# Optimization experiments

Hardware: AMD Instinct MI355X
Metric: run time of the kernel (lower is better)

## Reference

```python
import jax, jax.numpy as jnp
import numpy as np

EMBED_DIM = 1024
N_HEADS = 16

def setup_inputs() -> dict:
    key = jax.random.key(0)
    ks = jax.random.split(key, 5)
    C = EMBED_DIM
    std = 1.0 / np.sqrt(C)
    x = jax.random.normal(ks[0], (2, 2048, C), dtype=jnp.float32)
    w_attn = jax.random.normal(ks[1], (C, 3 * C), dtype=jnp.float32) * std  # (in, out)
    b_attn = jax.random.normal(ks[2], (3 * C,), dtype=jnp.float32) * 0.01
    w_proj = jax.random.normal(ks[3], (C, C), dtype=jnp.float32) * std
    b_proj = jax.random.normal(ks[4], (C,), dtype=jnp.float32) * 0.01
    return {"x": x, "w_attn": w_attn, "b_attn": b_attn, "w_proj": w_proj, "b_proj": b_proj}

def reference(x, w_attn, b_attn, w_proj, b_proj):
    B, T, C = x.shape
    H = N_HEADS
    D = C // H
    qkv = x @ w_attn + b_attn                      # (B, T, 3C)
    q, k, v = jnp.split(qkv, 3, axis=2)
    # (B, T, C) -> (B, H, T, D)
    q = q.reshape(B, T, H, D).transpose(0, 2, 1, 3)
    k = k.reshape(B, T, H, D).transpose(0, 2, 1, 3)
    v = v.reshape(B, T, H, D).transpose(0, 2, 1, 3)
    # Faithful to source: query is divided by scale BEFORE QK^T, and the
    # similarity is divided by scale AGAIN before softmax (net scale = 1/D).
    scale = jnp.asarray(D, dtype=x.dtype) ** 0.5
    q = q / scale
    sim = jnp.einsum('bhnd,bhsd->bhns', q, k)      # (B, H, T, T)
    causal = jnp.tril(jnp.ones((T, T), dtype=bool))
    neg_min = jnp.finfo(sim.dtype).min
    sim = jnp.where(causal[None, None, :, :], sim, neg_min)
    attn = jax.nn.softmax(sim / scale, axis=-1)
    out = jnp.einsum('bhns,bhsd->bhnd', attn, v)   # (B, H, T, D)
    # source: gqa returns (b n h d), forward does transpose(1,2) -> (b h n d)
    # then .view(B, T, C); net effect is reshaping the (B,H,T,D) layout.
    y = out.reshape(B, T, C)
    y = y @ w_proj + b_proj
    return y
```

## Files before the change

kernel.cpp:

```cpp
#include <hip/hip_runtime.h>
#include <hip/hip_bf16.h>

#define BB 2
#define TT 2048
#define CC 1024
#define HH 16
#define DD 64
#define MM (BB*TT)
#define QSZ ((size_t)MM*CC)

#define QSCALE 0.022542110013890053f

typedef __attribute__((ext_vector_type(8))) short bf16x8;
typedef __attribute__((ext_vector_type(4))) short bf16x4;
typedef __attribute__((ext_vector_type(4))) float f32x4;
typedef __attribute__((address_space(1))) const unsigned char as1_u8;
typedef __attribute__((address_space(3))) unsigned char as3_u8;

struct alignas(8) bf16x4_s { __hip_bfloat16 h[4]; };

static __device__ __forceinline__ f32x4 mfma16(bf16x4 a, bf16x4 b, f32x4 c) {
#if __has_builtin(__builtin_amdgcn_mfma_f32_16x16x16bf16_1k)
    return __builtin_amdgcn_mfma_f32_16x16x16bf16_1k(a, b, c, 0, 0, 0);
#else
    asm volatile("v_mfma_f32_16x16x16_bf16 %0, %1, %2, %0"
                 : "+v"(c) : "v"(a), "v"(b));
    return c;
#endif
}

static __device__ __forceinline__ short f2bf(float x) {
    __hip_bfloat16 h = __float2bfloat16(x);
    return *(short*)&h;
}

__constant__ unsigned char U_qi[48] = {
    15,31,30,31, 14,29,30,28,29, 13,27,28,26,27, 12,25,26,24,25,
    11,23,24,22,23, 10,21,22,20,21, 9,19,20,18,19, 8,17,18,16,17,
    7,16, 6,5,4,3,2,1,0};
__constant__ unsigned char U_t0[48] = {
    0,0,15,16, 0,0,0,14,15, 0,0,0,13,14, 0,0,0,12,13,
    0,0,0,11,12, 0,0,0,10,11, 0,0,0,9,10, 0,0,0,8,9,
    0,0, 0,0,0,0,0,0,0};
__constant__ unsigned char U_t1[48] = {
    16,16,31,32, 15,15,15,29,30, 14,14,14,27,28, 13,13,13,25,26,
    12,12,12,23,24, 11,11,11,21,22, 10,10,10,19,20, 9,9,9,17,18,
    8,8, 7,6,5,4,3,2,1};

__global__ __launch_bounds__(256) void convert_bf16(
    const float* __restrict__ in, __hip_bfloat16* __restrict__ outp, int n)
{
    const int i = (blockIdx.x * 256 + threadIdx.x) * 8;
    if (i + 8 <= n) {
        const float4 a = *(const float4*)&in[i];
        const float4 b = *(const float4*)&in[i + 4];
        __hip_bfloat16 tmp[8];
        tmp[0] = __float2bfloat16(a.x); tmp[1] = __float2bfloat16(a.y);
        tmp[2] = __float2bfloat16(a.z); tmp[3] = __float2bfloat16(a.w);
        tmp[4] = __float2bfloat16(b.x); tmp[5] = __float2bfloat16(b.y);
        tmp[6] = __float2bfloat16(b.z); tmp[7] = __float2bfloat16(b.w);
        *(float4*)&outp[i] = *(float4*)&tmp[0];
    }
}

__global__ __launch_bounds__(256) void transpose_convert(
    const float* __restrict__ in, __hip_bfloat16* __restrict__ outp, int R, int Cc)
{
    __shared__ float tile[64][68];
    const int c0 = blockIdx.x * 64, r0 = blockIdx.y * 64;
    const int t = threadIdx.x;
    {
        const int r = t >> 2, cb = (t & 3) * 16;
        #pragma unroll
        for (int i = 0; i < 4; ++i)
            *(float4*)&tile[r][cb + i*4] = *(const float4*)&in[(size_t)(r0 + r)*Cc + c0 + cb + i*4];
    }
    __syncthreads();
    {
        const int c = t >> 2, rb = (t & 3) * 16;
        __hip_bfloat16 tmp[16];
        #pragma unroll
        for (int j = 0; j < 16; ++j) tmp[j] = __float2bfloat16(tile[rb + j][c]);
        __hip_bfloat16* dst = outp + (size_t)(c0 + c)*R + r0 + rb;
        *(float4*)&dst[0] = *(float4*)&tmp[0];
        *(float4*)&dst[8] = *(float4*)&tmp[8];
    }
}

template<int MODE>
__global__ __launch_bounds__(256) void gemm_mfma(
    const __hip_bfloat16* __restrict__ A,
    const __hip_bfloat16* __restrict__ BT,
    const float* __restrict__ bias,
    void* __restrict__ out, int M, int N, int K)
{
    __shared__ __hip_bfloat16 As[128][64];
    __shared__ __hip_bfloat16 Bs[128][64];

    const int tid = threadIdx.x;
    const int w = tid >> 6, l = tid & 63;
    const int lr = l & 15, lg = l >> 4;
    const int wr = w >> 1, wc = w & 1;
    const int rsw = (lr & 7) << 4;
    const int lsw = ((l & 7) ^ (l >> 3)) * 8;

    const int nwg = gridDim.x * gridDim.y;
    const int bid = blockIdx.y * gridDim.x + blockIdx.x;
    const int swz_id = (bid & 7) * (nwg >> 3) + (bid >> 3);
    const int row0 = (swz_id / gridDim.x) * 128;
    const int col0 = (swz_id % gridDim.x) * 128;

    f32x4 acc[4][4] = {};

    for (int k0 = 0; k0 < K; k0 += 64) {
        __syncthreads();
        #pragma unroll
        for (int i = 0; i < 4; ++i) {
            const int br = w*32 + i*8;
            const __hip_bfloat16* ga = A  + (size_t)(row0 + br + (l>>3))*K + k0 + lsw;
            __builtin_amdgcn_global_load_lds((as1_u8*)ga, (as3_u8*)&As[br][0], 16, 0, 0);
            const __hip_bfloat16* gb = BT + (size_t)(col0 + br + (l>>3))*K + k0 + lsw;
            __builtin_amdgcn_global_load_lds((as1_u8*)gb, (as3_u8*)&Bs[br][0], 16, 0, 0);
        }
        __syncthreads();

        #pragma unroll
        for (int s = 0; s < 2; ++s) {
            bf16x8 af[4], bfr[4];
            #pragma unroll
            for (int m = 0; m < 4; ++m) {
                const char* ab = (const char*)&As[wr*64 + m*16 + lr][0];
                af[m] = *(const bf16x8*)(ab + ((s*64 + lg*16) ^ rsw));
            }
            #pragma unroll
            for (int n = 0; n < 4; ++n) {
                const char* bb = (const char*)&Bs[wc*64 + n*16 + lr][0];
                bfr[n] = *(const bf16x8*)(bb + ((s*64 + lg*16) ^ rsw));
            }
            #pragma unroll
            for (int m = 0; m < 4; ++m)
                #pragma unroll
                for (int n = 0; n < 4; ++n)
                    acc[m][n] = __builtin_amdgcn_mfma_f32_16x16x32_bf16(af[m], bfr[n], acc[m][n], 0, 0, 0);
        }
    }

    #pragma unroll
    for (int m = 0; m < 4; ++m) {
        #pragma unroll
        for (int n = 0; n < 4; ++n) {
            const int ng = col0 + wc*64 + n*16 + lr;
            const float bv = bias[ng];
            const int mg0 = row0 + wr*64 + m*16 + lg*4;
            if (MODE == 0) {
                const int which = ng >> 10, c = ng & 1023;
                const int h = c >> 6, d = c & 63;
                if (which == 2) {
                    const int b = mg0 >> 11, t0 = mg0 & 2047;
                    bf16x4_s pk;
                    #pragma unroll
                    for (int r = 0; r < 4; ++r)
                        pk.h[r] = __float2bfloat16(acc[m][n][r] + bv);
                    *(bf16x4_s*)((__hip_bfloat16*)out + (size_t)2*QSZ +
                        (((size_t)(b*HH + h))*DD + d)*TT + t0) = pk;
                } else {
                    #pragma unroll
                    for (int r = 0; r < 4; ++r) {
                        const int mg = mg0 + r;
                        float v = acc[m][n][r] + bv;
                        if (which == 0) v *= QSCALE;
                        const int b = mg >> 11, t = mg & 2047;
                        ((__hip_bfloat16*)out)[(size_t)which*QSZ +
                            (((size_t)(b*HH + h))*TT + t)*DD + d] = __float2bfloat16(v);
                    }
                }
            } else {
                #pragma unroll
                for (int r = 0; r < 4; ++r)
                    ((float*)out)[(size_t)(mg0 + r)*N + ng] = acc[m][n][r] + bv;
            }
        }
    }
}

__global__ __launch_bounds__(256) void attn_mfma(
    const __hip_bfloat16* __restrict__ Qb,
    const __hip_bfloat16* __restrict__ Kb,
    const __hip_bfloat16* __restrict__ Vb,
    __hip_bfloat16* __restrict__ Ob,
    __hip_bfloat16* __restrict__ Opart,
    float* __restrict__ Lpart)
{
    __shared__ __hip_bfloat16 k_lds[2][64][64];
    __shared__ __hip_bfloat16 vT[2][64][64];

    const int tid = threadIdx.x;
    const int w  = tid >> 6;
    const int l  = tid & 63;
    const int lr = l & 15;
    const int lg = l >> 4;
    const int swz = (lr & 7) << 4;

    const int bid = blockIdx.x;
    const int sid = (bid & 7) * 192 + (bid >> 3);
    const int bh  = sid / 48;
    const int u   = sid % 48;
    const int qi  = U_qi[u];
    const int t0i = U_t0[u];
    const int t1i = U_t1[u];
    const int qb  = qi * 64;

    const __hip_bfloat16* Qh = Qb + (size_t)bh*TT*DD;
    const __hip_bfloat16* Kh = Kb + (size_t)bh*TT*DD;
    const __hip_bfloat16* Vh = Vb + (size_t)bh*DD*TT;

    bf16x8 qa[2];
    const int qrow = qb + w*16 + lr;
    {
        const __hip_bfloat16* qp = Qh + (size_t)qrow*DD + lg*8;
        qa[0] = *(const bf16x8*)(qp);
        qa[1] = *(const bf16x8*)(qp + 32);
    }

    const int srow = tid >> 2, sch = tid & 3;
    const int wswz = (srow & 7) << 4;

    float4 kr0, kr1, vr0, vr1;
    {
        const __hip_bfloat16* ksrc = Kh + (size_t)(t0i*64 + srow)*DD + sch*16;
        const __hip_bfloat16* vsrc = Vh + (size_t)srow*TT + t0i*64 + sch*16;
        kr0 = *(const float4*)ksrc; kr1 = *(const float4*)(ksrc + 8);
        vr0 = *(const float4*)vsrc; vr1 = *(const float4*)(vsrc + 8);
    }
    {
        char* krow = (char*)&k_lds[0][srow][0];
        char* vrow = (char*)&vT[0][srow][0];
        *(float4*)(krow + ((sch*32)      ^ wswz)) = kr0;
        *(float4*)(krow + ((sch*32 + 16) ^ wswz)) = kr1;
        *(float4*)(vrow + ((sch*32)      ^ wswz)) = vr0;
        *(float4*)(vrow + ((sch*32 + 16) ^ wswz)) = vr1;
    }
    __syncthreads();

    f32x4 oacc[4] = {};
    float l_r = 0.f;

    int cur = 0;
    for (int t = t0i; t < t1i; ++t) {
        const int kv0 = t * 64;
        const bool has_next = (t + 1 < t1i);

        if (has_next) {
            const int kv1 = kv0 + 64;
            const __hip_bfloat16* ksrc = Kh + (size_t)(kv1 + srow)*DD + sch*16;
            const __hip_bfloat16* vsrc = Vh + (size_t)srow*TT + kv1 + sch*16;
            kr0 = *(const float4*)ksrc; kr1 = *(const float4*)(ksrc + 8);
            vr0 = *(const float4*)vsrc; vr1 = *(const float4*)(vsrc + 8);
        }

        f32x4 sacc[4] = {};
        #pragma unroll
        for (int mt = 0; mt < 4; ++mt) {
            const char* kbase = (const char*)&k_lds[cur][mt*16 + lr][0];
            const bf16x8 kb0 = *(const bf16x8*)(kbase + ((     16*lg) ^ swz));
            const bf16x8 kb1 = *(const bf16x8*)(kbase + ((64 + 16*lg) ^ swz));
            sacc[mt] = __builtin_amdgcn_mfma_f32_16x16x32_bf16(kb0, qa[0], sacc[mt], 0, 0, 0);
            sacc[mt] = __builtin_amdgcn_mfma_f32_16x16x32_bf16(kb1, qa[1], sacc[mt], 0, 0, 0);
        }

        if (t == qi) {
            #pragma unroll
            for (int mt = 0; mt < 4; ++mt)
                #pragma unroll
                for (int r = 0; r < 4; ++r)
                    if (kv0 + mt*16 + lg*4 + r > qrow) sacc[mt][r] = -3.0e38f;
        }
        bf16x4 pk[4];
        #pragma unroll
        for (int mt = 0; mt < 4; ++mt) {
            float p0 = exp2f(sacc[mt][0]), p1 = exp2f(sacc[mt][1]);
            float p2 = exp2f(sacc[mt][2]), p3 = exp2f(sacc[mt][3]);
            l_r += (p0 + p1) + (p2 + p3);
            pk[mt][0] = f2bf(p0); pk[mt][1] = f2bf(p1);
            pk[mt][2] = f2bf(p2); pk[mt][3] = f2bf(p3);
        }

        #pragma unroll
        for (int dt = 0; dt < 4; ++dt) {
            const char* vbase = (const char*)&vT[cur][dt*16 + lr][0];
            #pragma unroll
            for (int mt = 0; mt < 4; ++mt) {
                const bf16x4 vb = *(const bf16x4*)(vbase + ((mt*32 + lg*8) ^ swz));
                oacc[dt] = mfma16(vb, pk[mt], oacc[dt]);
            }
        }

        if (has_next) {
            char* krow = (char*)&k_lds[cur ^ 1][srow][0];
            char* vrow = (char*)&vT[cur ^ 1][srow][0];
            *(float4*)(krow + ((sch*32)      ^ wswz)) = kr0;
            *(float4*)(krow + ((sch*32 + 16) ^ wswz)) = kr1;
            *(float4*)(vrow + ((sch*32)      ^ wswz)) = vr0;
            *(float4*)(vrow + ((sch*32 + 16) ^ wswz)) = vr1;
            __syncthreads();
            cur ^= 1;
        }
    }

    l_r += __shfl_xor(l_r, 16);
    l_r += __shfl_xor(l_r, 32);

    if (qi >= 16) {
        const int s = (t0i != 0);
        const int unit = ((bh*16 + (qi - 16)) << 1) | s;
        const int rowu = w*16 + lr;
        __hip_bfloat16* Oprow = Opart + ((size_t)unit*64 + rowu)*64;
        #pragma unroll
        for (int dt = 0; dt < 4; ++dt) {
            bf16x4_s ok;
            #pragma unroll
            for (int r = 0; r < 4; ++r)
                ok.h[r] = __float2bfloat16(oacc[dt][r]);
            *(bf16x4_s*)(Oprow + dt*16 + lg*4) = ok;
        }
        if (lg == 0) Lpart[unit*64 + rowu] = l_r;
    } else {
        __hip_bfloat16* Orow = Ob + ((size_t)bh*TT + qrow)*DD;
        const float inv = 1.0f / l_r;
        #pragma unroll
        for (int dt = 0; dt < 4; ++dt) {
            bf16x4_s ok;
            #pragma unroll
            for (int r = 0; r < 4; ++r)
                ok.h[r] = __float2bfloat16(oacc[dt][r] * inv);
            *(bf16x4_s*)(Orow + dt*16 + lg*4) = ok;
        }
    }
}

__global__ __launch_bounds__(256) void attn_combine(
    const __hip_bfloat16* __restrict__ Opart,
    const float* __restrict__ Lpart,
    __hip_bfloat16* __restrict__ Ob)
{
    const int w = threadIdx.x >> 6, d = threadIdx.x & 63;
    const int rowg = blockIdx.x * 4 + w;
    const int r  = rowg & 63;
    const int jj = (rowg >> 6) & 15;
    const int bh = rowg >> 10;
    const int u0 = (bh*16 + jj) << 1;
    const float inv = 1.0f / (Lpart[u0*64 + r] + Lpart[(u0 + 1)*64 + r]);
    const float o1 = __bfloat162float(Opart[((size_t)u0*64 + r)*64 + d]);
    const float o2 = __bfloat162float(Opart[((size_t)(u0 + 1)*64 + r)*64 + d]);
    const int qrow = (16 + jj)*64 + r;
    Ob[((size_t)bh*TT + qrow)*DD + d] = __float2bfloat16((o1 + o2) * inv);
}

extern "C" void kernel_launch(void* const* d_in, const int* in_sizes, int n_in,
                              void* d_out, int out_size, void* d_ws, size_t ws_size,
                              hipStream_t stream)
{
    const float* x      = (const float*)d_in[0];
    const float* w_attn = (const float*)d_in[1];
    const float* b_attn = (const float*)d_in[2];
    const float* w_proj = (const float*)d_in[3];
    const float* b_proj = (const float*)d_in[4];
    float* out = (float*)d_out;

    __hip_bfloat16* xb     = (__hip_bfloat16*)d_ws;
    __hip_bfloat16* wqkvT  = xb + QSZ;
    __hip_bfloat16* wprojT = wqkvT + 3*CC*CC;
    __hip_bfloat16* Qb     = wprojT + CC*CC;
    __hip_bfloat16* Kb     = Qb + QSZ;
    __hip_bfloat16* Vt     = Kb + QSZ;
    __hip_bfloat16* Ob     = Vt + QSZ;

    __hip_bfloat16* Opart  = xb;
    float*          Lpart  = (float*)wqkvT;

    convert_bf16<<<dim3(QSZ/(256*8)), 256, 0, stream>>>(x, xb, (int)QSZ);
    transpose_convert<<<dim3(3*CC/64, CC/64), 256, 0, stream>>>(w_attn, wqkvT, CC, 3*CC);
    transpose_convert<<<dim3(CC/64, CC/64), 256, 0, stream>>>(w_proj, wprojT, CC, CC);

    gemm_mfma<0><<<dim3(3*CC/128, MM/128), 256, 0, stream>>>(xb, wqkvT, b_attn, (void*)Qb, MM, 3*CC, CC);

    attn_mfma<<<dim3(32*48), 256, 0, stream>>>(Qb, Kb, Vt, Ob, Opart, Lpart);

    attn_combine<<<dim3(32768/4), 256, 0, stream>>>(Opart, Lpart, Ob);

    gemm_mfma<1><<<dim3(CC/128, MM/128), 256, 0, stream>>>(Ob, wprojT, b_proj, (void*)out, MM, CC, CC);
}
```

Baseline: 123.7 us.

## Read K and V tiles directly from global memory instead of staging in LDS

The attention kernel drops its double-buffered LDS staging of K and V tiles and the per-tile block barrier. Each wave now loads its MFMA operands for K and transposed V straight from global memory, relying on the L1/L2 caches to serve the reuse across the four waves. This removes LDS writes, the swizzle arithmetic and the __syncthreads, but gives up explicit prefetch overlap. Every wave now issues its own, possibly less coalesced, global loads for the same data.

```diff
diff --git a/kernel.cpp b/kernel.cpp
--- a/kernel.cpp
+++ b/kernel.cpp
@@ -191,15 +191,11 @@
     __hip_bfloat16* __restrict__ Opart,
     float* __restrict__ Lpart)
 {
-    __shared__ __hip_bfloat16 k_lds[2][64][64];
-    __shared__ __hip_bfloat16 vT[2][64][64];
-
     const int tid = threadIdx.x;
     const int w  = tid >> 6;
     const int l  = tid & 63;
     const int lr = l & 15;
     const int lg = l >> 4;
-    const int swz = (lr & 7) << 4;
 
     const int bid = blockIdx.x;
     const int sid = (bid & 7) * 192 + (bid >> 3);
@@ -222,48 +218,21 @@
         qa[1] = *(const bf16x8*)(qp + 32);
     }
 
-    const int srow = tid >> 2, sch = tid & 3;
-    const int wswz = (srow & 7) << 4;
-
-    float4 kr0, kr1, vr0, vr1;
-    {
-        const __hip_bfloat16* ksrc = Kh + (size_t)(t0i*64 + srow)*DD + sch*16;
-        const __hip_bfloat16* vsrc = Vh + (size_t)srow*TT + t0i*64 + sch*16;
-        kr0 = *(const float4*)ksrc; kr1 = *(const float4*)(ksrc + 8);
-        vr0 = *(const float4*)vsrc; vr1 = *(const float4*)(vsrc + 8);
-    }
-    {
-        char* krow = (char*)&k_lds[0][srow][0];
-        char* vrow = (char*)&vT[0][srow][0];
-        *(float4*)(krow + ((sch*32)      ^ wswz)) = kr0;
-        *(float4*)(krow + ((sch*32 + 16) ^ wswz)) = kr1;
-        *(float4*)(vrow + ((sch*32)      ^ wswz)) = vr0;
-        *(float4*)(vrow + ((sch*32 + 16) ^ wswz)) = vr1;
-    }
-    __syncthreads();
+    const __hip_bfloat16* kbase = Kh + (size_t)lr*DD + lg*8;
+    const __hip_bfloat16* vbase = Vh + (size_t)lr*TT + lg*4;
 
     f32x4 oacc[4] = {};
     float l_r = 0.f;
 
-    int cur = 0;
     for (int t = t0i; t < t1i; ++t) {
         const int kv0 = t * 64;
-        const bool has_next = (t + 1 < t1i);
-
-        if (has_next) {
-            const int kv1 = kv0 + 64;
-            const __hip_bfloat16* ksrc = Kh + (size_t)(kv1 + srow)*DD + sch*16;
-            const __hip_bfloat16* vsrc = Vh + (size_t)srow*TT + kv1 + sch*16;
-            kr0 = *(const float4*)ksrc; kr1 = *(const float4*)(ksrc + 8);
-            vr0 = *(const float4*)vsrc; vr1 = *(const float4*)(vsrc + 8);
-        }
 
         f32x4 sacc[4] = {};
         #pragma unroll
         for (int mt = 0; mt < 4; ++mt) {
-            const char* kbase = (const char*)&k_lds[cur][mt*16 + lr][0];
-            const bf16x8 kb0 = *(const bf16x8*)(kbase + ((     16*lg) ^ swz));
-            const bf16x8 kb1 = *(const bf16x8*)(kbase + ((64 + 16*lg) ^ swz));
+            const __hip_bfloat16* kp = kbase + (size_t)(kv0 + mt*16)*DD;
+            const bf16x8 kb0 = *(const bf16x8*)kp;
+            const bf16x8 kb1 = *(const bf16x8*)(kp + 32);
             sacc[mt] = __builtin_amdgcn_mfma_f32_16x16x32_bf16(kb0, qa[0], sacc[mt], 0, 0, 0);
             sacc[mt] = __builtin_amdgcn_mfma_f32_16x16x32_bf16(kb1, qa[1], sacc[mt], 0, 0, 0);
         }
@@ -287,23 +256,12 @@
 
         #pragma unroll
         for (int dt = 0; dt < 4; ++dt) {
-            const char* vbase = (const char*)&vT[cur][dt*16 + lr][0];
+            const __hip_bfloat16* vp = vbase + (size_t)(dt*16)*TT + kv0;
             #pragma unroll
             for (int mt = 0; mt < 4; ++mt) {
-                const bf16x4 vb = *(const bf16x4*)(vbase + ((mt*32 + lg*8) ^ swz));
+                const bf16x4 vb = *(const bf16x4*)(vp + mt*16);
                 oacc[dt] = mfma16(vb, pk[mt], oacc[dt]);
             }
-        }
-
-        if (has_next) {
-            char* krow = (char*)&k_lds[cur ^ 1][srow][0];
-            char* vrow = (char*)&vT[cur ^ 1][srow][0];
-            *(float4*)(krow + ((sch*32)      ^ wswz)) = kr0;
-            *(float4*)(krow + ((sch*32 + 16) ^ wswz)) = kr1;
-            *(float4*)(vrow + ((sch*32)      ^ wswz)) = vr0;
-            *(float4*)(vrow + ((sch*32 + 16) ^ wswz)) = vr1;
-            __syncthreads();
-            cur ^= 1;
         }
     }
 
```

Result: slower. 287.5 us (+132.4%).
